# Kernel optimization log

Hardware: AMD Instinct MI355X
Metric: run time of the kernel (lower is better)

## Reference

```python
import jax, jax.numpy as jnp
import numpy as np

B, S, D, H = 2, 2048, 1024, 16
DK = D // H

def setup_inputs() -> dict:
    key = jax.random.key(0)
    ks = jax.random.split(key, 12)
    s = 0.02
    inp = {
        'query': jax.random.normal(ks[0], (B, S, D), jnp.float32),
        'key':   jax.random.normal(ks[1], (B, S, D), jnp.float32),
        'value': jax.random.normal(ks[2], (B, S, D), jnp.float32),
        'mask':  jnp.broadcast_to(jnp.tril(jnp.ones((S, S), jnp.int32)), (B, S, S)),
        'wq': jax.random.normal(ks[3], (D, D), jnp.float32) * s,
        'bq': jnp.zeros((D,), jnp.float32),
        'wk': jax.random.normal(ks[4], (D, D), jnp.float32) * s,
        'bk': jnp.zeros((D,), jnp.float32),
        'wv': jax.random.normal(ks[5], (D, D), jnp.float32) * s,
        'bv': jnp.zeros((D,), jnp.float32),
        'wo': jax.random.normal(ks[6], (D, D), jnp.float32) * s,
        'bo': jnp.zeros((D,), jnp.float32),
    }
    return inp

def reference(query, key, value, mask, wq, bq, wk, bk, wv, bv, wo, bo):
    # Linear projections (torch Linear: x @ W.T + b); W stored (out,in)
    Q = query @ wq.T + bq   # (B,Sq,D)
    K = key   @ wk.T + bk   # (B,Sk,D)
    V = value @ wv.T + bv   # (B,Sk,D)
    # split heads -> (B,H,S,DK)
    Q = Q.reshape(B, S, H, DK).transpose(0, 2, 1, 3)
    K = K.reshape(B, S, H, DK).transpose(0, 2, 1, 3)
    V = V.reshape(B, S, H, DK).transpose(0, 2, 1, 3)
    scores = jnp.einsum('bhqd,bhkd->bhqk', Q, K) / jnp.sqrt(jnp.float32(DK))
    scores = jnp.where(mask[:, None, :, :] == 0, -jnp.inf, scores)
    attn = jax.nn.softmax(scores, axis=-1)  # dropout is identity in eval/reference
    context = jnp.einsum('bhqk,bhkd->bhqd', attn, V)
    context = context.transpose(0, 2, 1, 3).reshape(B, S, D)
    return context @ wo.T + bo
```

## Files before the change

### kernel.cpp

```cpp
#include <hip/hip_runtime.h>
#include <hip/hip_bf16.h>


#define B_ 2
#define S_ 2048
#define D_ 1024
#define H_ 16
#define DK_ 64
#define SZX (4096 * 1024)
#define SZW (1024 * 1024)

typedef __attribute__((ext_vector_type(8))) short short8;
typedef __attribute__((ext_vector_type(4))) float f32x4;

using bf16 = __hip_bfloat16;

__device__ __forceinline__ short8 load8(const bf16* p) {
    return *reinterpret_cast<const short8*>(p);
}

__device__ __forceinline__ f32x4 mfma16(short8 a, short8 b, f32x4 c) {
    return __builtin_amdgcn_mfma_f32_16x16x32_bf16(a, b, c, 0, 0, 0);
}

__device__ __forceinline__ void async16(const bf16* g, bf16* l) {
    __builtin_amdgcn_global_load_lds(
        (const __attribute__((address_space(1))) void*)g,
        (__attribute__((address_space(3))) void*)l, 16, 0, 0);
}

__device__ __forceinline__ short bf16rne(float f) {
    unsigned u = __float_as_uint(f);
    return (short)((u + 0x7FFFu + ((u >> 16) & 1u)) >> 16);
}

struct CvtArgs {
    const float* src[7];
    bf16* dst[7];
};

__global__ __launch_bounds__(256) void cvt_kernel(CvtArgs a) {
    const long long e = ((long long)blockIdx.x * 256 + threadIdx.x) * 8;
    int t; long long off;
    if (e < 3LL * SZX) { t = (int)(e >> 22); off = e & (SZX - 1); }
    else { const long long e2 = e - 3LL * SZX; t = 3 + (int)(e2 >> 20); off = e2 & (SZW - 1); }
    const float4 f0 = *reinterpret_cast<const float4*>(a.src[t] + off);
    const float4 f1 = *reinterpret_cast<const float4*>(a.src[t] + off + 4);
    short8 o;
    o[0] = bf16rne(f0.x); o[1] = bf16rne(f0.y); o[2] = bf16rne(f0.z); o[3] = bf16rne(f0.w);
    o[4] = bf16rne(f1.x); o[5] = bf16rne(f1.y); o[6] = bf16rne(f1.z); o[7] = bf16rne(f1.w);
    *reinterpret_cast<short8*>((short*)a.dst[t] + off) = o;
}

struct ProjArgs {
    const bf16* X[3]; const bf16* W[3]; const float* bias[3]; void* Y[3]; int mode[3];
};

template <int BM>
__global__ __launch_bounds__(256) void proj_kernel(ProjArgs a) {
    const int z = blockIdx.z;
    const bf16* __restrict__ X = a.X[z];
    const bf16* __restrict__ W = a.W[z];
    const float* __restrict__ bias = a.bias[z];
    const int mode = a.mode[z];

    constexpr int MSUB = BM / 32;
    __shared__ __align__(16) bf16 lA[BM * 64];
    __shared__ __align__(16) bf16 lB[128 * 64];

    const int tid  = threadIdx.x;
    const int wv   = tid >> 6;
    const int lane = tid & 63;
    const int quad = lane >> 4;
    const int l16  = lane & 15;
    const int m0   = blockIdx.x * BM;
    const int n0   = blockIdx.y * 128;
    const int wm   = (wv & 1) * (BM / 2);
    const int wn   = (wv >> 1) * 64;

    const int srow  = wv * 8 + (lane >> 3);
    const int sunit = (lane & 7) ^ ((lane >> 3) & 7);
    const bf16* gA = X + (size_t)(m0 + srow) * D_ + sunit * 8;
    const bf16* gB = W + (size_t)(n0 + srow) * D_ + sunit * 8;

    f32x4 acc[MSUB][4] = {};

    #pragma unroll 1
    for (int k0 = 0; k0 < D_; k0 += 64) {
        #pragma unroll
        for (int c = 0; c < MSUB; ++c)
            async16(gA + (size_t)c * 32 * D_ + k0, &lA[(c * 32 + wv * 8) * 64]);
        #pragma unroll
        for (int c = 0; c < 4; ++c)
            async16(gB + (size_t)c * 32 * D_ + k0, &lB[(c * 32 + wv * 8) * 64]);
        __syncthreads();
        #pragma unroll
        for (int kh = 0; kh < 2; ++kh) {
            short8 af[MSUB], bf_[4];
            #pragma unroll
            for (int ms = 0; ms < MSUB; ++ms)
                af[ms] = load8(&lA[(wm + ms * 16 + l16) * 64 + (((kh * 4 + quad) ^ (l16 & 7)) * 8)]);
            #pragma unroll
            for (int ns = 0; ns < 4; ++ns)
                bf_[ns] = load8(&lB[(wn + ns * 16 + l16) * 64 + (((kh * 4 + quad) ^ (l16 & 7)) * 8)]);
            #pragma unroll
            for (int ms = 0; ms < MSUB; ++ms)
                #pragma unroll
                for (int ns = 0; ns < 4; ++ns)
                    acc[ms][ns] = mfma16(af[ms], bf_[ns], acc[ms][ns]);
        }
        __syncthreads();
    }

    #pragma unroll
    for (int ns = 0; ns < 4; ++ns) {
        const int col = n0 + wn + ns * 16 + l16;
        const float bv = bias[col];
        const int h = col >> 6, d = col & 63;
        #pragma unroll
        for (int ms = 0; ms < MSUB; ++ms) {
            const int rbase = m0 + wm + ms * 16 + quad * 4;
            #pragma unroll
            for (int r = 0; r < 4; ++r) {
                const int m = rbase + r;
                const float val = acc[ms][ns][r] + bv;
                if (mode == 3) {
                    ((float*)a.Y[z])[(size_t)m * D_ + col] = val;
                } else {
                    bf16* Y = (bf16*)a.Y[z];
                    const bf16 o = __float2bfloat16(val);
                    const int b  = m >> 11;
                    const int s  = m & (S_ - 1);
                    const int bh = b * H_ + h;
                    if (mode == 2) Y[((size_t)bh * DK_ + d) * S_ + s] = o;
                    else           Y[((size_t)bh * S_ + s) * DK_ + d] = o;
                }
            }
        }
    }
}

__global__ __launch_bounds__(256) void attn_kernel(
    const bf16* __restrict__ Qb, const bf16* __restrict__ Kb,
    const bf16* __restrict__ Vt, bf16* __restrict__ ctx)
{
    __shared__ __align__(16) bf16 Kt[64 * 64];
    __shared__ __align__(16) bf16 Vl[64 * 64];
    __shared__ __align__(16) bf16 lds_p[4][16][72];

    const int tid  = threadIdx.x;
    const int wv   = tid >> 6;
    const int lane = tid & 63;
    const int quad = lane >> 4;
    const int l16  = lane & 15;

    const int bx = blockIdx.x;
    const int bh = (bx & 7) * 4 + ((bx >> 3) & 3);
    const int m  = 31 - (bx >> 5);
    const int q0 = m * 64;
    const int qr = q0 + wv * 16;

    const bf16* Qh = Qb + (size_t)bh * (S_ * DK_);
    const bf16* Kh = Kb + (size_t)bh * (S_ * DK_);
    const bf16* Vh = Vt + (size_t)bh * (DK_ * S_);

    const float c = 0.18033688011112042f;
    const short8 ones = {16256, 16256, 16256, 16256, 16256, 16256, 16256, 16256};

    const int srow  = wv * 8 + (lane >> 3);
    const int sunit = (lane & 7) ^ ((lane >> 3) & 7);

    const short8 qa0 = load8(Qh + (qr + l16) * DK_ + quad * 8);
    const short8 qa1 = load8(Qh + (qr + l16) * DK_ + 32 + quad * 8);

    f32x4 cacc[4] = {};
    f32x4 lsum = {};

    for (int jt = 0; jt <= m; ++jt) {
        const int j0 = jt * 64;

        #pragma unroll
        for (int cc = 0; cc < 2; ++cc) {
            const int r = cc * 32 + srow;
            async16(Kh + (size_t)(j0 + r) * DK_ + sunit * 8, &Kt[(cc * 32 + wv * 8) * 64]);
            async16(Vh + (size_t)r * S_ + j0 + sunit * 8,    &Vl[(cc * 32 + wv * 8) * 64]);
        }
        __syncthreads();

        short8 kb[4][2], vb[4][2];
        #pragma unroll
        for (int t = 0; t < 4; ++t)
            #pragma unroll
            for (int kh = 0; kh < 2; ++kh) {
                const int u = ((kh * 4 + quad) ^ (l16 & 7)) * 8;
                kb[t][kh] = load8(&Kt[(t * 16 + l16) * 64 + u]);
                vb[t][kh] = load8(&Vl[(t * 16 + l16) * 64 + u]);
            }

        f32x4 s[4];
        #pragma unroll
        for (int t = 0; t < 4; ++t) {
            f32x4 zz = {};
            zz = mfma16(qa0, kb[t][0], zz);
            s[t] = mfma16(qa1, kb[t][1], zz);
        }

        if (jt < m) {
            #pragma unroll
            for (int r = 0; r < 4; ++r)
                #pragma unroll
                for (int t = 0; t < 4; ++t)
                    lds_p[wv][quad * 4 + r][t * 16 + l16] =
                        __float2bfloat16(exp2f(c * s[t][r]));
        } else {
            #pragma unroll
            for (int r = 0; r < 4; ++r) {
                const int row = qr + quad * 4 + r;
                #pragma unroll
                for (int t = 0; t < 4; ++t) {
                    const float p = (j0 + t * 16 + l16 <= row) ? exp2f(c * s[t][r]) : 0.f;
                    lds_p[wv][quad * 4 + r][t * 16 + l16] = __float2bfloat16(p);
                }
            }
        }

        asm volatile("s_waitcnt lgkmcnt(0)" ::: "memory");
        const short8 pa0 = load8(&lds_p[wv][l16][quad * 8]);
        const short8 pa1 = load8(&lds_p[wv][l16][32 + quad * 8]);

        #pragma unroll
        for (int dt = 0; dt < 4; ++dt) {
            cacc[dt] = mfma16(pa0, vb[dt][0], cacc[dt]);
            cacc[dt] = mfma16(pa1, vb[dt][1], cacc[dt]);
        }
        lsum = mfma16(pa0, ones, lsum);
        lsum = mfma16(pa1, ones, lsum);

        __syncthreads();
    }

    const int bb = bh >> 4, hh = bh & 15;
    #pragma unroll
    for (int r = 0; r < 4; ++r) {
        const float inv = 1.0f / lsum[r];
        const int row = qr + quad * 4 + r;
        bf16* orow = ctx + (size_t)(bb * S_ + row) * D_ + hh * DK_;
        #pragma unroll
        for (int dt = 0; dt < 4; ++dt)
            orow[dt * 16 + l16] = __float2bfloat16(cacc[dt][r] * inv);
    }
}

extern "C" void kernel_launch(void* const* d_in, const int* in_sizes, int n_in,
                              void* d_out, int out_size, void* d_ws, size_t ws_size,
                              hipStream_t stream) {
    (void)in_sizes; (void)n_in; (void)out_size; (void)ws_size;
    const float* q  = (const float*)d_in[0];
    const float* k  = (const float*)d_in[1];
    const float* v  = (const float*)d_in[2];
    const float* wq = (const float*)d_in[4];
    const float* bq = (const float*)d_in[5];
    const float* wk = (const float*)d_in[6];
    const float* bk = (const float*)d_in[7];
    const float* wv = (const float*)d_in[8];
    const float* bv = (const float*)d_in[9];
    const float* wo = (const float*)d_in[10];
    const float* bo = (const float*)d_in[11];

    bf16* base = (bf16*)d_ws;
    bf16* Qb  = base;
    bf16* Kb  = base + 1 * (size_t)SZX;
    bf16* Vt  = base + 2 * (size_t)SZX;
    bf16* ctx = base + 3 * (size_t)SZX;
    bf16* xq  = base + 4 * (size_t)SZX;
    bf16* xk  = base + 5 * (size_t)SZX;
    bf16* xv  = base + 6 * (size_t)SZX;
    bf16* wqb = base + 7 * (size_t)SZX;
    bf16* wkb = wqb + 1 * (size_t)SZW;
    bf16* wvb = wqb + 2 * (size_t)SZW;
    bf16* wob = wqb + 3 * (size_t)SZW;

    CvtArgs ca;
    ca.src[0] = q;  ca.src[1] = k;  ca.src[2] = v;
    ca.src[3] = wq; ca.src[4] = wk; ca.src[5] = wv; ca.src[6] = wo;
    ca.dst[0] = xq;  ca.dst[1] = xk;  ca.dst[2] = xv;
    ca.dst[3] = wqb; ca.dst[4] = wkb; ca.dst[5] = wvb; ca.dst[6] = wob;
    cvt_kernel<<<8192, 256, 0, stream>>>(ca);

    ProjArgs pa;
    pa.X[0] = xq;  pa.X[1] = xk;  pa.X[2] = xv;
    pa.W[0] = wqb; pa.W[1] = wkb; pa.W[2] = wvb;
    pa.bias[0] = bq; pa.bias[1] = bk; pa.bias[2] = bv;
    pa.Y[0] = Qb; pa.Y[1] = Kb; pa.Y[2] = Vt;
    pa.mode[0] = 0; pa.mode[1] = 1; pa.mode[2] = 2;
    proj_kernel<128><<<dim3(32, 8, 3), 256, 0, stream>>>(pa);

    attn_kernel<<<dim3(1024), 256, 0, stream>>>(Qb, Kb, Vt, ctx);

    ProjArgs po;
    po.X[0] = ctx; po.W[0] = wob; po.bias[0] = bo; po.Y[0] = d_out; po.mode[0] = 3;
    po.X[1] = ctx; po.W[1] = wob; po.bias[1] = bo; po.Y[1] = d_out; po.mode[1] = 3;
    po.X[2] = ctx; po.W[2] = wob; po.bias[2] = bo; po.Y[2] = d_out; po.mode[2] = 3;
    proj_kernel<64><<<dim3(64, 8, 1), 256, 0, stream>>>(po);
}
```

Baseline: 249.8 us.

## Switch projection GEMM to 32x32x16 MFMA with fragment-ordered LDS layout

Rewrites the projection GEMM inner loop to use the 32x32x16 bf16 MFMA instead of 16x16x32. The LDS tiles are restructured so that each 32-row by 16-k fragment is stored contiguously in lane order, which lets each lane do a single linear 16-byte read with no XOR swizzle. The larger MFMA raises the ratio of math to LDS traffic per instruction. The trade-off is a different output register layout in the epilogue and possible bank conflicts on the async global-to-LDS writes.

```diff
diff --git a/kernel.cpp b/kernel.cpp
--- a/kernel.cpp
+++ b/kernel.cpp
@@ -12,6 +12,7 @@
 
 typedef __attribute__((ext_vector_type(8))) short short8;
 typedef __attribute__((ext_vector_type(4))) float f32x4;
+typedef __attribute__((ext_vector_type(16))) float f32x16;
 
 using bf16 = __hip_bfloat16;
 
@@ -21,6 +22,10 @@
 
 __device__ __forceinline__ f32x4 mfma16(short8 a, short8 b, f32x4 c) {
     return __builtin_amdgcn_mfma_f32_16x16x32_bf16(a, b, c, 0, 0, 0);
+}
+
+__device__ __forceinline__ f32x16 mfma32(short8 a, short8 b, f32x16 c) {
+    return __builtin_amdgcn_mfma_f32_32x32x16_bf16(a, b, c, 0, 0, 0);
 }
 
 __device__ __forceinline__ void async16(const bf16* g, bf16* l) {
@@ -58,72 +63,76 @@
 
 template <int BM>
 __global__ __launch_bounds__(256) void proj_kernel(ProjArgs a) {
+    constexpr int MSUB = BM / 32;
+    constexpr int WM   = MSUB / 2;
+
     const int z = blockIdx.z;
     const bf16* __restrict__ X = a.X[z];
     const bf16* __restrict__ W = a.W[z];
     const float* __restrict__ bias = a.bias[z];
     const int mode = a.mode[z];
 
-    constexpr int MSUB = BM / 32;
-    __shared__ __align__(16) bf16 lA[BM * 64];
-    __shared__ __align__(16) bf16 lB[128 * 64];
+    __shared__ __align__(16) bf16 lA[MSUB * 4 * 512];
+    __shared__ __align__(16) bf16 lB[16 * 512];
 
     const int tid  = threadIdx.x;
     const int wv   = tid >> 6;
     const int lane = tid & 63;
-    const int quad = lane >> 4;
-    const int l16  = lane & 15;
+    const int l31  = lane & 31;
+    const int khi  = lane >> 5;
     const int m0   = blockIdx.x * BM;
     const int n0   = blockIdx.y * 128;
-    const int wm   = (wv & 1) * (BM / 2);
-    const int wn   = (wv >> 1) * 64;
-
-    const int srow  = wv * 8 + (lane >> 3);
-    const int sunit = (lane & 7) ^ ((lane >> 3) & 7);
-    const bf16* gA = X + (size_t)(m0 + srow) * D_ + sunit * 8;
-    const bf16* gB = W + (size_t)(n0 + srow) * D_ + sunit * 8;
-
-    f32x4 acc[MSUB][4] = {};
+
+    const bf16* gA[MSUB];
+    #pragma unroll
+    for (int s = 0; s < MSUB; ++s) {
+        const int fa = wv * MSUB + s;
+        gA[s] = X + (size_t)(m0 + (fa >> 2) * 32 + l31) * D_ + (fa & 3) * 16 + khi * 8;
+    }
+    const bf16* gB = W + (size_t)(n0 + wv * 32 + l31) * D_ + khi * 8;
+
+    f32x16 acc[WM][2] = {};
 
     #pragma unroll 1
     for (int k0 = 0; k0 < D_; k0 += 64) {
         #pragma unroll
-        for (int c = 0; c < MSUB; ++c)
-            async16(gA + (size_t)c * 32 * D_ + k0, &lA[(c * 32 + wv * 8) * 64]);
-        #pragma unroll
-        for (int c = 0; c < 4; ++c)
-            async16(gB + (size_t)c * 32 * D_ + k0, &lB[(c * 32 + wv * 8) * 64]);
+        for (int s = 0; s < MSUB; ++s)
+            async16(gA[s] + k0, &lA[(wv * MSUB + s) * 512]);
+        #pragma unroll
+        for (int s = 0; s < 4; ++s)
+            async16(gB + k0 + s * 16, &lB[(wv * 4 + s) * 512]);
         __syncthreads();
-        #pragma unroll
-        for (int kh = 0; kh < 2; ++kh) {
-            short8 af[MSUB], bf_[4];
-            #pragma unroll
-            for (int ms = 0; ms < MSUB; ++ms)
-                af[ms] = load8(&lA[(wm + ms * 16 + l16) * 64 + (((kh * 4 + quad) ^ (l16 & 7)) * 8)]);
-            #pragma unroll
-            for (int ns = 0; ns < 4; ++ns)
-                bf_[ns] = load8(&lB[(wn + ns * 16 + l16) * 64 + (((kh * 4 + quad) ^ (l16 & 7)) * 8)]);
-            #pragma unroll
-            for (int ms = 0; ms < MSUB; ++ms)
+
+        #pragma unroll
+        for (int kk = 0; kk < 4; ++kk) {
+            short8 af[WM], bfr[2];
+            #pragma unroll
+            for (int mi = 0; mi < WM; ++mi)
+                af[mi] = load8(&lA[(((wv & 1) * WM + mi) * 4 + kk) * 512 + lane * 8]);
+            #pragma unroll
+            for (int ni = 0; ni < 2; ++ni)
+                bfr[ni] = load8(&lB[(((wv >> 1) * 2 + ni) * 4 + kk) * 512 + lane * 8]);
+            #pragma unroll
+            for (int mi = 0; mi < WM; ++mi)
                 #pragma unroll
-                for (int ns = 0; ns < 4; ++ns)
-                    acc[ms][ns] = mfma16(af[ms], bf_[ns], acc[ms][ns]);
+                for (int ni = 0; ni < 2; ++ni)
+                    acc[mi][ni] = mfma32(af[mi], bfr[ni], acc[mi][ni]);
         }
         __syncthreads();
     }
 
     #pragma unroll
-    for (int ns = 0; ns < 4; ++ns) {
-        const int col = n0 + wn + ns * 16 + l16;
+    for (int ni = 0; ni < 2; ++ni) {
+        const int col = n0 + (wv >> 1) * 64 + ni * 32 + l31;
         const float bv = bias[col];
         const int h = col >> 6, d = col & 63;
         #pragma unroll
-        for (int ms = 0; ms < MSUB; ++ms) {
-            const int rbase = m0 + wm + ms * 16 + quad * 4;
-            #pragma unroll
-            for (int r = 0; r < 4; ++r) {
-                const int m = rbase + r;
-                const float val = acc[ms][ns][r] + bv;
+        for (int mi = 0; mi < WM; ++mi) {
+            const int rb = m0 + ((wv & 1) * WM + mi) * 32 + 4 * khi;
+            #pragma unroll
+            for (int reg = 0; reg < 16; ++reg) {
+                const int m = rb + (reg & 3) + 8 * (reg >> 2);
+                const float val = acc[mi][ni][reg] + bv;
                 if (mode == 3) {
                     ((float*)a.Y[z])[(size_t)m * D_ + col] = val;
                 } else {
```

New measurement: 278.5 us. +11.5%, slower.
